# Optimization experiments

Measured on AMD Instinct MI355X. Metric: run time of the kernel, lower is better.

Reference implementation:

```python
import jax, jax.numpy as jnp
import numpy as np

NUM_HEADS = 8


def _mab(Q, K, Wq, bq, Wk, bk, Wv, bv, Wo, bo):
    # MAB with ln=False, dropout=0 (eval). Scale is sqrt(dim_V), matching source.
    B, Lq, _ = Q.shape
    Lk = K.shape[1]
    Dv = Wq.shape[1]
    dh = Dv // NUM_HEADS
    q = (Q @ Wq + bq).reshape(B, Lq, NUM_HEADS, dh).transpose(0, 2, 1, 3)
    k = (K @ Wk + bk).reshape(B, Lk, NUM_HEADS, dh).transpose(0, 2, 1, 3)
    v = (K @ Wv + bv).reshape(B, Lk, NUM_HEADS, dh).transpose(0, 2, 1, 3)
    A = jax.nn.softmax(jnp.einsum('bhqd,bhkd->bhqk', q, k) / jnp.sqrt(jnp.float32(Dv)), axis=-1)
    O = (q + jnp.einsum('bhqk,bhkd->bhqd', A, v)).transpose(0, 2, 1, 3).reshape(B, Lq, Dv)
    return O + jax.nn.relu(O @ Wo + bo)


def _forward(x, adj, gin_W, gin_b, geW1, geb1, geW2, geb2,
             gnW1, gnb1, gnW2, gnb2, goW, gob, S,
             mWq, mbq, mWk, mbk, mWv, mbv, mWo, mbo, finW, finb):
    B, V, T, D = x.shape
    Hd = gin_W.shape[1]
    # --- GNN encoder (adj path) ---
    h = x.reshape(B, V, T * D) @ gin_W + gin_b            # [B,V,H]
    # edge_mlp first linear on cat([h_i,h_j]) == h@Wi (row) + h@Wj (col); avoids 2H concat
    Wi, Wj = geW1[:Hd], geW1[Hd:]
    pre = (h @ Wi)[:, :, None, :] + (h @ Wj)[:, None, :, :] + geb1   # [B,V,V,H]
    e = jax.nn.relu(jax.nn.relu(pre) @ geW2 + geb2)       # [B,V,V,H]
    agg = jnp.einsum('bijh,bij->bih', e, adj)             # mask * sum over j, fused
    node = jax.nn.relu(jax.nn.relu(agg @ gnW1 + gnb1) @ gnW2 + gnb2)
    enc = node @ goW + gob                                # [B,V,H]
    # --- decoder: PMA + SAB + SAB + Linear ---
    o = _mab(jnp.broadcast_to(S, (B,) + S.shape[1:]), enc,
             mWq[0], mbq[0], mWk[0], mbk[0], mWv[0], mbv[0], mWo[0], mbo[0])
    o = _mab(o, o, mWq[1], mbq[1], mWk[1], mbk[1], mWv[1], mbv[1], mWo[1], mbo[1])
    o = _mab(o, o, mWq[2], mbq[2], mWk[2], mbk[2], mWv[2], mbv[2], mWo[2], mbo[2])
    out = o @ finW + finb                                 # [B,num_slots,T*OD]
    return out.reshape(B, S.shape[1], T, finW.shape[1] // T)


def setup_inputs() -> dict:
    key = jax.random.key(0)
    ks = jax.random.split(key, 16)
    B, V, T, D = 4, 256, 12, 4
    H, NS, OD = 256, 16, 32

    def w(k, shape, s=0.02):
        return s * jax.random.normal(k, shape, jnp.float32)

    return {
        'x': jax.random.normal(ks[0], (B, V, T, D), jnp.float32),
        'adj': (jax.random.uniform(ks[1], (B, V, V)) > 0.5).astype(jnp.float32),
        'gin_W': w(ks[2], (T * D, H)), 'gin_b': jnp.zeros((H,), jnp.float32),
        'geW1': w(ks[3], (2 * H, H)), 'geb1': jnp.zeros((H,), jnp.float32),
        'geW2': w(ks[4], (H, H)), 'geb2': jnp.zeros((H,), jnp.float32),
        'gnW1': w(ks[5], (H, H)), 'gnb1': jnp.zeros((H,), jnp.float32),
        'gnW2': w(ks[6], (H, H)), 'gnb2': jnp.zeros((H,), jnp.float32),
        'goW': w(ks[7], (H, H)), 'gob': jnp.zeros((H,), jnp.float32),
        'S': w(ks[8], (1, NS, H), 0.05),
        'mWq': w(ks[9], (3, H, H)), 'mbq': jnp.zeros((3, H), jnp.float32),
        'mWk': w(ks[10], (3, H, H)), 'mbk': jnp.zeros((3, H), jnp.float32),
        'mWv': w(ks[11], (3, H, H)), 'mbv': jnp.zeros((3, H), jnp.float32),
        'mWo': w(ks[12], (3, H, H)), 'mbo': jnp.zeros((3, H), jnp.float32),
        'finW': w(ks[13], (H, T * OD)), 'finb': jnp.zeros((T * OD,), jnp.float32),
    }


def reference(x, adj, gin_W, gin_b, geW1, geb1, geW2, geb2,
              gnW1, gnb1, gnW2, gnb2, goW, gob, S,
              mWq, mbq, mWk, mbk, mWv, mbv, mWo, mbo, finW, finb):
    return _forward(x, adj, gin_W, gin_b, geW1, geb1, geW2, geb2,
                    gnW1, gnb1, gnW2, gnb2, goW, gob, S,
                    mWq, mbq, mWk, mbk, mWv, mbv, mWo, mbo, finW, finb)
```

## Files before the change

### kernel.cpp

```cpp
#include <hip/hip_runtime.h>
#include <hip/hip_bf16.h>

typedef unsigned short u16;
typedef __bf16 bf8v __attribute__((ext_vector_type(8)));
typedef float f4v __attribute__((ext_vector_type(4)));

__device__ __forceinline__ float b2f(u16 v) {
  union { unsigned u; float f; } x; x.u = ((unsigned)v) << 16; return x.f;
}
__device__ __forceinline__ u16 f2b(float f) {
  union { float f; unsigned u; } x; x.f = f;
  unsigned r = (x.u + 0x7FFFu + ((x.u >> 16) & 1u)) >> 16;
  return (u16)r;
}
__device__ __forceinline__ unsigned pkbf(float a, float b) {
  union { __hip_bfloat162 h; unsigned u; } c;
  c.h = __float22bfloat162_rn(make_float2(a, b));
  return c.u;
}
__device__ __forceinline__ void up2(unsigned u, float& lo, float& hi) {
  union { unsigned x; float f; } a, b;
  a.x = u << 16; b.x = u & 0xffff0000u; lo = a.f; hi = b.f;
}

#define NFRAG 19
struct PreArgs {
  const float* fsrc[NFRAG];
  u16* fdst[NFRAG];
  int fstride[NFRAG];
  int fbase[NFRAG + 1];
  int fragTiles, hBase, prepBid, q1Bid;
  const float *x, *ginW, *ginb;
  u16* h_bf;
  const float *mbk, *mbv, *mbq, *S, *mWq;
  float *bkv0, *bqkv1, *bqkv2;
  u16* q1b;
};

__global__ __launch_bounds__(256) void k_pre(PreArgs a) {
  __shared__ u16 ld[256 * 20];
  __shared__ float xs[4][48];
  __shared__ float Ss[4096];
  const int bid = blockIdx.x, t = threadIdx.x;

  if (bid < a.fragTiles) {
    int j = 0;
    while (j + 1 < NFRAG && a.fbase[j + 1] <= bid) j++;
    const int localT = bid - a.fbase[j];
    const float* src = a.fsrc[j];
    const int Ns = a.fstride[j];
    const int n0 = localT * 16;
    {
      const float* s = src + (size_t)t * Ns + n0;
      const float4 v0 = ((const float4*)s)[0], v1 = ((const float4*)s)[1];
      const float4 v2 = ((const float4*)s)[2], v3 = ((const float4*)s)[3];
      unsigned* row = (unsigned*)(ld + t * 20);
      row[0] = pkbf(v0.x, v0.y); row[1] = pkbf(v0.z, v0.w);
      row[2] = pkbf(v1.x, v1.y); row[3] = pkbf(v1.z, v1.w);
      row[4] = pkbf(v2.x, v2.y); row[5] = pkbf(v2.z, v2.w);
      row[6] = pkbf(v3.x, v3.y); row[7] = pkbf(v3.z, v3.w);
    }
    __syncthreads();
    u16* dst = a.fdst[j] + (size_t)localT * 4096;
#pragma unroll
    for (int s2 = 0; s2 < 2; s2++) {
      const int o = t * 2 + s2, kt = o >> 6, lane = o & 63;
      const int nlo = lane & 15, bk = kt * 32 + ((lane >> 4) << 3);
      union { u16 h[8]; uint4 q; } pk;
#pragma unroll
      for (int j2 = 0; j2 < 8; j2++) pk.h[j2] = ld[(bk + j2) * 20 + nlo];
      *(uint4*)(dst + (size_t)(kt * 64 + lane) * 8) = pk.q;
    }
    return;
  }
  if (bid >= a.hBase && bid < a.hBase + 256) {
    const int row0 = (bid - a.hBase) * 4;
    if (t < 192) {
      const int rr = t / 48, k = t % 48;
      xs[rr][k] = a.x[(size_t)(row0 + rr) * 48 + k];
    }
    __syncthreads();
    const float bias = a.ginb[t];
    float acc[4] = {bias, bias, bias, bias};
    for (int k = 0; k < 48; k++) {
      const float w = a.ginW[(size_t)k * 256 + t];
#pragma unroll
      for (int rr = 0; rr < 4; rr++) acc[rr] += xs[rr][k] * w;
    }
#pragma unroll
    for (int rr = 0; rr < 4; rr++) a.h_bf[(size_t)(row0 + rr) * 256 + t] = f2b(acc[rr]);
    return;
  }
  if (bid == a.prepBid) {
    a.bkv0[t] = a.mbk[t]; a.bkv0[256 + t] = a.mbv[t];
    a.bqkv1[t] = a.mbq[256 + t]; a.bqkv1[256 + t] = a.mbk[256 + t]; a.bqkv1[512 + t] = a.mbv[256 + t];
    a.bqkv2[t] = a.mbq[512 + t]; a.bqkv2[256 + t] = a.mbk[512 + t]; a.bqkv2[512 + t] = a.mbv[512 + t];
    return;
  }
  if (bid == a.q1Bid) {
    for (int idx = t; idx < 4096; idx += 256) Ss[idx] = a.S[idx];
    __syncthreads();
    float acc[16];
#pragma unroll
    for (int r = 0; r < 16; r++) acc[r] = 0.f;
    for (int k = 0; k < 256; k++) {
      const float w = a.mWq[(size_t)k * 256 + t];
#pragma unroll
      for (int r = 0; r < 16; r++) acc[r] += Ss[r * 256 + k] * w;
    }
    const float bq = a.mbq[t];
#pragma unroll
    for (int r = 0; r < 16; r++) a.q1b[r * 256 + t] = f2b(acc[r] + bq);
    return;
  }
}

__global__ __launch_bounds__(256) void k_wiwj(
    const u16* __restrict__ h, const u16* __restrict__ frag, float* __restrict__ out) {
  __shared__ __align__(16) u16 As[64 * 264];
  const int t = threadIdx.x, lane = t & 63, wv = t >> 6;
  const int m0 = blockIdx.x * 64, n0 = blockIdx.y * 128;
  {
    const int row = t >> 2, ch = t & 3;
#pragma unroll
    for (int s = 0; s < 8; s++)
      *(uint4*)(As + row * 264 + ch * 64 + s * 8) =
          *(const uint4*)(h + (size_t)(m0 + row) * 256 + ch * 64 + s * 8);
  }
  __syncthreads();
  f4v acc[4][2];
#pragma unroll
  for (int mt = 0; mt < 4; mt++)
#pragma unroll
    for (int nt = 0; nt < 2; nt++) acc[mt][nt] = (f4v){0.f, 0.f, 0.f, 0.f};
  const int Tw = (n0 >> 4) + wv * 2;
#pragma unroll
  for (int kt = 0; kt < 8; kt++) {
    bf8v af[4], bf[2];
#pragma unroll
    for (int mt = 0; mt < 4; mt++)
      af[mt] = *(const bf8v*)(As + (mt * 16 + (lane & 15)) * 264 + kt * 32 + ((lane >> 4) << 3));
#pragma unroll
    for (int nt = 0; nt < 2; nt++)
      bf[nt] = *(const bf8v*)(frag + ((size_t)((Tw + nt) * 8 + kt) * 64 + lane) * 8);
#pragma unroll
    for (int mt = 0; mt < 4; mt++)
#pragma unroll
      for (int nt = 0; nt < 2; nt++)
        acc[mt][nt] = __builtin_amdgcn_mfma_f32_16x16x32_bf16(af[mt], bf[nt], acc[mt][nt], 0, 0, 0);
  }
#pragma unroll
  for (int mt = 0; mt < 4; mt++)
#pragma unroll
    for (int nt = 0; nt < 2; nt++) {
      const int n = n0 + wv * 32 + nt * 16 + (lane & 15);
      const int mb = m0 + mt * 16 + ((lane >> 4) << 2);
#pragma unroll
      for (int r = 0; r < 4; r++) out[(size_t)(mb + r) * 512 + n] = acc[mt][nt][r];
    }
}

__global__ __launch_bounds__(256, 2) void k_edge(
    const float* __restrict__ hWiWj, const float* __restrict__ adj,
    const float* __restrict__ geb1, const u16* __restrict__ fragW2,
    const float* __restrict__ geb2, u16* __restrict__ aggB) {
  __shared__ __align__(16) u16 As[64 * 264];
  __shared__ float hi[256];
  __shared__ int jlist[256];
  __shared__ int cnt;
  const int t = threadIdx.x, lane = t & 63, wv = t >> 6;
  const int b = blockIdx.x >> 8, i = blockIdx.x & 255;
  if (t == 0) cnt = 0;
  __syncthreads();
  {
    const float a = adj[(size_t)(b * 256 + i) * 256 + t];
    hi[t] = hWiWj[(size_t)(b * 256 + i) * 512 + t] + geb1[t];
    if (a != 0.f) { const int p = atomicAdd(&cnt, 1); jlist[p] = t; }
  }
  __syncthreads();
  const int nact = cnt;
  if (nact == 0) {
    if (lane < 16) {
#pragma unroll
      for (int nt = 0; nt < 4; nt++)
        aggB[(size_t)(b * 256 + i) * 256 + wv * 64 + nt * 16 + lane] = 0;
    }
    return;
  }
  const int nch = (nact + 63) >> 6;
  float bias2[4];
#pragma unroll
  for (int nt = 0; nt < 4; nt++) bias2[nt] = geb2[wv * 64 + nt * 16 + (lane & 15)];
  float aggAcc[4] = {0.f, 0.f, 0.f, 0.f};
  const u16* fw = fragW2 + lane * 8;

  for (int c = 0; c < nch; c++) {
    const int rows = min(64, nact - c * 64);
    {
      const int r = t >> 2, q = t & 3;
      const bool valid = (r < rows);
      const int j = valid ? jlist[c * 64 + r] : jlist[0];
      const float4* s4 = (const float4*)(hWiWj + (size_t)(b * 256 + j) * 512 + 256 + q * 64);
      u16* dstrow = As + r * 264 + q * 64;
#pragma unroll
      for (int ii = 0; ii < 8; ii++) {
        const float4 v0 = s4[ii * 2];
        const float4 v1 = s4[ii * 2 + 1];
        const int k = q * 64 + ii * 8;
        uint4 qd;
        qd.x = pkbf(fmaxf(v0.x + hi[k + 0], 0.f), fmaxf(v0.y + hi[k + 1], 0.f));
        qd.y = pkbf(fmaxf(v0.z + hi[k + 2], 0.f), fmaxf(v0.w + hi[k + 3], 0.f));
        qd.z = pkbf(fmaxf(v1.x + hi[k + 4], 0.f), fmaxf(v1.y + hi[k + 5], 0.f));
        qd.w = pkbf(fmaxf(v1.z + hi[k + 6], 0.f), fmaxf(v1.w + hi[k + 7], 0.f));
        *(uint4*)(dstrow + ii * 8) = qd;
      }
    }
    __syncthreads();
    f4v acc[4][4];
#pragma unroll
    for (int jt = 0; jt < 4; jt++)
#pragma unroll
      for (int nt = 0; nt < 4; nt++) acc[jt][nt] = (f4v){0.f, 0.f, 0.f, 0.f};
    bf8v bcur[4];
#pragma unroll
    for (int nt = 0; nt < 4; nt++)
      bcur[nt] = *(const bf8v*)(fw + (size_t)((wv * 4 + nt) * 8 + 0) * 512);
#pragma unroll
    for (int kt = 0; kt < 8; kt++) {
      bf8v bnxt[4];
      if (kt < 7) {
#pragma unroll
        for (int nt = 0; nt < 4; nt++)
          bnxt[nt] = *(const bf8v*)(fw + (size_t)((wv * 4 + nt) * 8 + kt + 1) * 512);
      }
      bf8v af[4];
#pragma unroll
      for (int jt = 0; jt < 4; jt++)
        af[jt] = *(const bf8v*)(As + (jt * 16 + (lane & 15)) * 264 + kt * 32 + ((lane >> 4) << 3));
#pragma unroll
      for (int nt = 0; nt < 4; nt++)
#pragma unroll
        for (int jt = 0; jt < 4; jt++)
          acc[jt][nt] = __builtin_amdgcn_mfma_f32_16x16x32_bf16(af[jt], bcur[nt], acc[jt][nt], 0, 0, 0);
      if (kt < 7) {
#pragma unroll
        for (int nt = 0; nt < 4; nt++) bcur[nt] = bnxt[nt];
      }
    }
    const int rbase = (lane >> 4) * 4;
#pragma unroll
    for (int nt = 0; nt < 4; nt++) {
      float s = 0.f;
#pragma unroll
      for (int jt = 0; jt < 4; jt++) {
        const int r0 = jt * 16 + rbase;
#pragma unroll
        for (int r = 0; r < 4; r++) {
          const float e = fmaxf(acc[jt][nt][r] + bias2[nt], 0.f);
          s += (r0 + r < rows) ? e : 0.f;
        }
      }
      s += __shfl_xor(s, 16);
      s += __shfl_xor(s, 32);
      aggAcc[nt] += s;
    }
    __syncthreads();
  }
  if (lane < 16) {
#pragma unroll
    for (int nt = 0; nt < 4; nt++) {
      const int n = wv * 64 + nt * 16 + lane;
      aggB[(size_t)(b * 256 + i) * 256 + n] = f2b(aggAcc[nt]);
    }
  }
}

#define NBLK 32

__device__ __forceinline__ void gridbar(int* cnt, int gen) {
  __syncthreads();
  if (threadIdx.x == 0) {
    __threadfence();
    __hip_atomic_fetch_add(cnt, 1, __ATOMIC_RELAXED, __HIP_MEMORY_SCOPE_AGENT);
    int it = 0;
    while (__hip_atomic_load(cnt, __ATOMIC_RELAXED, __HIP_MEMORY_SCOPE_AGENT) < NBLK * gen) {
      __builtin_amdgcn_s_sleep(8);
      if (((++it) & 255) == 0)
        __hip_atomic_fetch_add(cnt, 0, __ATOMIC_RELAXED, __HIP_MEMORY_SCOPE_AGENT);
    }
    __threadfence();
  }
  __syncthreads();
}

__device__ void g32(const u16* Al, const u16* frag, const float* bias, int relu,
                    u16* Ol, int t) {
  const int lane = t & 63, wv = t >> 6;
  f4v acc[2][4];
#pragma unroll
  for (int mt = 0; mt < 2; mt++)
#pragma unroll
    for (int nt = 0; nt < 4; nt++) acc[mt][nt] = (f4v){0.f, 0.f, 0.f, 0.f};
#pragma unroll
  for (int kt = 0; kt < 8; kt++) {
    bf8v af[2], bf[4];
#pragma unroll
    for (int mt = 0; mt < 2; mt++)
      af[mt] = *(const bf8v*)(Al + (mt * 16 + (lane & 15)) * 264 + kt * 32 + ((lane >> 4) << 3));
#pragma unroll
    for (int nt = 0; nt < 4; nt++)
      bf[nt] = *(const bf8v*)(frag + ((size_t)((wv * 4 + nt) * 8 + kt) * 64 + lane) * 8);
#pragma unroll
    for (int mt = 0; mt < 2; mt++)
#pragma unroll
      for (int nt = 0; nt < 4; nt++)
        acc[mt][nt] = __builtin_amdgcn_mfma_f32_16x16x32_bf16(af[mt], bf[nt], acc[mt][nt], 0, 0, 0);
  }
#pragma unroll
  for (int mt = 0; mt < 2; mt++)
#pragma unroll
    for (int nt = 0; nt < 4; nt++) {
      const int col = wv * 64 + nt * 16 + (lane & 15);
      const float bv = bias[col];
#pragma unroll
      for (int r = 0; r < 4; r++) {
        const int row = mt * 16 + ((lane >> 4) << 2) + r;
        float v = acc[mt][nt][r] + bv;
        if (relu) v = fmaxf(v, 0.f);
        Ol[row * 264 + col] = f2b(v);
      }
    }
}

__device__ void g32kv(const u16* Al, const u16* frag, const float* bias,
                      u16* outG, int t) {
  const int lane = t & 63, wv = t >> 6;
  f4v acc[2][8];
#pragma unroll
  for (int mt = 0; mt < 2; mt++)
#pragma unroll
    for (int nt = 0; nt < 8; nt++) acc[mt][nt] = (f4v){0.f, 0.f, 0.f, 0.f};
#pragma unroll
  for (int kt = 0; kt < 8; kt++) {
    bf8v af[2];
#pragma unroll
    for (int mt = 0; mt < 2; mt++)
      af[mt] = *(const bf8v*)(Al + (mt * 16 + (lane & 15)) * 264 + kt * 32 + ((lane >> 4) << 3));
#pragma unroll
    for (int nt = 0; nt < 8; nt++) {
      const bf8v bf = *(const bf8v*)(frag + ((size_t)((wv * 8 + nt) * 8 + kt) * 64 + lane) * 8);
#pragma unroll
      for (int mt = 0; mt < 2; mt++)
        acc[mt][nt] = __builtin_amdgcn_mfma_f32_16x16x32_bf16(af[mt], bf, acc[mt][nt], 0, 0, 0);
    }
  }
#pragma unroll
  for (int mt = 0; mt < 2; mt++)
#pragma unroll
    for (int nt = 0; nt < 8; nt++) {
      const int col = wv * 128 + nt * 16 + (lane & 15);
      const float bv = bias[col];
#pragma unroll
      for (int r = 0; r < 4; r++) {
        const int row = mt * 16 + ((lane >> 4) << 2) + r;
        outG[(size_t)row * 512 + col] = f2b(acc[mt][nt][r] + bv);
      }
    }
}

__device__ void wproj(const u16* __restrict__ actA, const float* __restrict__ residG,
                      const u16* __restrict__ frag, const float* __restrict__ bias,
                      int mode, u16* __restrict__ outBf, float* __restrict__ outF,
                      int Nout, int b, int T, int lane) {
  f4v acc = (f4v){0.f, 0.f, 0.f, 0.f};
  const u16* abase = actA + (size_t)(b * 16 + (lane & 15)) * 256 + ((lane >> 4) << 3);
  const u16* fbase = frag + ((size_t)(T * 8) * 64 + lane) * 8;
#pragma unroll
  for (int kt = 0; kt < 8; kt++) {
    const bf8v af = *(const bf8v*)(abase + kt * 32);
    const bf8v bf = *(const bf8v*)(fbase + (size_t)kt * 512);
    acc = __builtin_amdgcn_mfma_f32_16x16x32_bf16(af, bf, acc, 0, 0, 0);
  }
  const int col = T * 16 + (lane & 15);
  const float bv = bias[col];
#pragma unroll
  for (int r = 0; r < 4; r++) {
    const int row = b * 16 + ((lane >> 4) << 2) + r;
    float v = acc[r] + bv;
    if (mode == 1) v = fmaxf(v, 0.f) + residG[(size_t)row * 256 + col];
    if (outBf) outBf[(size_t)row * Nout + col] = f2b(v);
    if (outF) outF[(size_t)row * Nout + col] = v;
  }
}

__device__ void wattn(const u16* __restrict__ qkvG, float* __restrict__ attF,
                      u16* __restrict__ attB, float* psW, int b, int hd, int lane) {
  const int r = lane & 15, cg = lane >> 4;
  float qv[32];
  {
    const uint4* qp = (const uint4*)(qkvG + (size_t)(b * 16 + r) * 768 + hd * 32);
#pragma unroll
    for (int c4 = 0; c4 < 4; c4++) {
      const uint4 q4 = qp[c4];
      up2(q4.x, qv[c4 * 8 + 0], qv[c4 * 8 + 1]);
      up2(q4.y, qv[c4 * 8 + 2], qv[c4 * 8 + 3]);
      up2(q4.z, qv[c4 * 8 + 4], qv[c4 * 8 + 5]);
      up2(q4.w, qv[c4 * 8 + 6], qv[c4 * 8 + 7]);
    }
  }
  float p[4];
#pragma unroll
  for (int c = 0; c < 4; c++) {
    const int cc = cg * 4 + c;
    const uint4* kp = (const uint4*)(qkvG + (size_t)(b * 16 + cc) * 768 + 256 + hd * 32);
    float s = 0.f;
#pragma unroll
    for (int c4 = 0; c4 < 4; c4++) {
      const uint4 k4 = kp[c4];
      float k0, k1;
      up2(k4.x, k0, k1); s += qv[c4 * 8 + 0] * k0 + qv[c4 * 8 + 1] * k1;
      up2(k4.y, k0, k1); s += qv[c4 * 8 + 2] * k0 + qv[c4 * 8 + 3] * k1;
      up2(k4.z, k0, k1); s += qv[c4 * 8 + 4] * k0 + qv[c4 * 8 + 5] * k1;
      up2(k4.w, k0, k1); s += qv[c4 * 8 + 6] * k0 + qv[c4 * 8 + 7] * k1;
    }
    p[c] = s * 0.0625f;
  }
  float mx = fmaxf(fmaxf(p[0], p[1]), fmaxf(p[2], p[3]));
  mx = fmaxf(mx, __shfl_xor(mx, 16));
  mx = fmaxf(mx, __shfl_xor(mx, 32));
  float sum = 0.f;
#pragma unroll
  for (int c = 0; c < 4; c++) { p[c] = __expf(p[c] - mx); sum += p[c]; }
  sum += __shfl_xor(sum, 16);
  sum += __shfl_xor(sum, 32);
  const float inv = 1.f / sum;
#pragma unroll
  for (int c = 0; c < 4; c++) psW[r * 16 + cg * 4 + c] = p[c] * inv;
  float o[8];
#pragma unroll
  for (int j = 0; j < 8; j++) o[j] = qv[cg * 8 + j];
#pragma unroll
  for (int c = 0; c < 16; c++) {
    const float pv = psW[r * 16 + c];
    const uint4 v4 = *(const uint4*)(qkvG + (size_t)(b * 16 + c) * 768 + 512 + hd * 32 + cg * 8);
    float v0, v1;
    up2(v4.x, v0, v1); o[0] += pv * v0; o[1] += pv * v1;
    up2(v4.y, v0, v1); o[2] += pv * v0; o[3] += pv * v1;
    up2(v4.z, v0, v1); o[4] += pv * v0; o[5] += pv * v1;
    up2(v4.w, v0, v1); o[6] += pv * v0; o[7] += pv * v1;
  }
  const int row = b * 16 + r, col0 = hd * 32 + cg * 8;
#pragma unroll
  for (int j = 0; j < 8; j++) attF[(size_t)row * 256 + col0 + j] = o[j];
  unsigned* ob = (unsigned*)(attB + (size_t)row * 256 + col0);
  ob[0] = pkbf(o[0], o[1]); ob[1] = pkbf(o[2], o[3]);
  ob[2] = pkbf(o[4], o[5]); ob[3] = pkbf(o[6], o[7]);
}

__device__ void attn_tile(const u16* __restrict__ qbuf, int qshared,
                          const u16* __restrict__ kbuf, const u16* __restrict__ vbuf,
                          float* __restrict__ oF, u16* __restrict__ oB,
                          int b, int hd, float* qs, float* sc, float* vs, int t) {
  const int lane = t & 63, wv = t >> 6;
  const int Lk = 256;
  if (t < 64) {
    const int row = t >> 2, part = t & 3;
    const int qrow = qshared ? row : (b * 16 + row);
    const uint4 q4 = *(const uint4*)(qbuf + (size_t)qrow * 256 + hd * 32 + part * 8);
    float f0, f1, f2, f3, f4, f5, f6, f7;
    up2(q4.x, f0, f1); up2(q4.y, f2, f3); up2(q4.z, f4, f5); up2(q4.w, f6, f7);
    float4* d = (float4*)(qs + row * 32 + part * 8);
    d[0] = make_float4(f0, f1, f2, f3);
    d[1] = make_float4(f4, f5, f6, f7);
  }
  __syncthreads();
  {
    float kv[32];
    const uint4* kp = (const uint4*)(kbuf + (size_t)(b * Lk + t) * 512 + hd * 32);
#pragma unroll
    for (int c4 = 0; c4 < 4; c4++) {
      const uint4 k4 = kp[c4];
      up2(k4.x, kv[c4 * 8 + 0], kv[c4 * 8 + 1]);
      up2(k4.y, kv[c4 * 8 + 2], kv[c4 * 8 + 3]);
      up2(k4.z, kv[c4 * 8 + 4], kv[c4 * 8 + 5]);
      up2(k4.w, kv[c4 * 8 + 6], kv[c4 * 8 + 7]);
    }
    for (int r = 0; r < 16; r++) {
      float s = 0.f;
#pragma unroll
      for (int d = 0; d < 32; d++) s += qs[r * 32 + d] * kv[d];
      sc[r * 256 + t] = s * 0.0625f;
    }
  }
  __syncthreads();
  for (int r = wv * 4; r < wv * 4 + 4; r++) {
    float v[4];
    float mx = -1e30f;
#pragma unroll
    for (int q2 = 0; q2 < 4; q2++) {
      v[q2] = sc[r * 256 + lane + q2 * 64];
      mx = fmaxf(mx, v[q2]);
    }
    for (int off = 32; off; off >>= 1) mx = fmaxf(mx, __shfl_xor(mx, off));
    float sum = 0.f;
#pragma unroll
    for (int q2 = 0; q2 < 4; q2++) { v[q2] = __expf(v[q2] - mx); sum += v[q2]; }
    for (int off = 32; off; off >>= 1) sum += __shfl_xor(sum, off);
    const float inv = 1.f / sum;
#pragma unroll
    for (int q2 = 0; q2 < 4; q2++) sc[r * 256 + lane + q2 * 64] = v[q2] * inv;
  }
  __syncthreads();
  for (int u = t; u < 1024; u += 256) {
    const int row = u >> 2, part = u & 3;
    const uint4 v4 = *(const uint4*)(vbuf + (size_t)(b * Lk + row) * 512 + hd * 32 + part * 8);
    float f0, f1, f2, f3, f4, f5, f6, f7;
    up2(v4.x, f0, f1); up2(v4.y, f2, f3); up2(v4.z, f4, f5); up2(v4.w, f6, f7);
    float4* d = (float4*)(vs + row * 32 + part * 8);
    d[0] = make_float4(f0, f1, f2, f3);
    d[1] = make_float4(f4, f5, f6, f7);
  }
  __syncthreads();
  const int r0 = t >> 5, d = t & 31;
  float a0 = qs[r0 * 32 + d], a1 = qs[(r0 + 8) * 32 + d];
#pragma unroll 4
  for (int j = 0; j < Lk; j++) {
    const float vv = vs[j * 32 + d];
    a0 += sc[r0 * 256 + j] * vv;
    a1 += sc[(r0 + 8) * 256 + j] * vv;
  }
  const int c0 = hd * 32 + d;
  oF[(size_t)(b * 16 + r0) * 256 + c0] = a0;
  oB[(size_t)(b * 16 + r0) * 256 + c0] = f2b(a0);
  oF[(size_t)(b * 16 + r0 + 8) * 256 + c0] = a1;
  oB[(size_t)(b * 16 + r0 + 8) * 256 + c0] = f2b(a1);
}

struct TailArgs {
  const u16 *agg, *fGn1, *fGn2, *fGo, *fKV0, *fQKV1, *fQKV2, *fO0, *fO1, *fO2, *fFin, *q1b;
  const float *gnb1, *gnb2, *gob, *bkv0, *bqkv1, *bqkv2, *mbo, *finb;
  u16 *kv1, *o1b, *actBf, *qkvG, *attB;
  float *o1f, *attF, *outF;
  int* bar;
};

__global__ __launch_bounds__(256) void k_tail(TailArgs a) {
  __shared__ __align__(16) char smem[51200];
  const int bid = blockIdx.x, t = threadIdx.x;
  const int lane = t & 63;
  const int wid = bid * 4 + (t >> 6);

  {
    u16* actA = (u16*)smem;
    u16* actB = (u16*)(smem + 16896);
    const int r0 = bid * 32;
#pragma unroll
    for (int s = 0; s < 4; s++) {
      const int u = t * 4 + s, row = u >> 5, ch = u & 31;
      *(uint4*)(actA + row * 264 + ch * 8) =
          *(const uint4*)(a.agg + (size_t)(r0 + row) * 256 + ch * 8);
    }
    __syncthreads();
    g32(actA, a.fGn1, a.gnb1, 1, actB, t); __syncthreads();
    g32(actB, a.fGn2, a.gnb2, 1, actA, t); __syncthreads();
    g32(actA, a.fGo, a.gob, 0, actB, t); __syncthreads();
    g32kv(actB, a.fKV0, a.bkv0, a.kv1 + (size_t)r0 * 512, t);
  }
  gridbar(a.bar, 1);
  {
    float* qs = (float*)smem;
    float* sc = (float*)(smem + 2048);
    float* vs = (float*)(smem + 18432);
    attn_tile(a.q1b, 1, a.kv1, a.kv1 + 256, a.o1f, a.o1b, bid >> 3, bid & 7, qs, sc, vs, t);
  }
  gridbar(a.bar, 2);
  float* psW = (float*)smem + (t >> 6) * 256;
  if (wid < 64) wproj(a.o1b, a.o1f, a.fO0, a.mbo, 1, a.actBf, nullptr, 256, wid >> 4, wid & 15, lane);
  gridbar(a.bar, 3);
  for (int u = wid; u < 192; u += 128)
    wproj(a.actBf, nullptr, a.fQKV1, a.bqkv1, 0, a.qkvG, nullptr, 768, u / 48, u % 48, lane);
  gridbar(a.bar, 4);
  if (wid < 32) wattn(a.qkvG, a.attF, a.attB, psW, wid >> 3, wid & 7, lane);
  gridbar(a.bar, 5);
  if (wid < 64) wproj(a.attB, a.attF, a.fO1, a.mbo + 256, 1, a.actBf, nullptr, 256, wid >> 4, wid & 15, lane);
  gridbar(a.bar, 6);
  for (int u = wid; u < 192; u += 128)
    wproj(a.actBf, nullptr, a.fQKV2, a.bqkv2, 0, a.qkvG, nullptr, 768, u / 48, u % 48, lane);
  gridbar(a.bar, 7);
  if (wid < 32) wattn(a.qkvG, a.attF, a.attB, psW, wid >> 3, wid & 7, lane);
  gridbar(a.bar, 8);
  if (wid < 64) wproj(a.attB, a.attF, a.fO2, a.mbo + 512, 1, a.actBf, nullptr, 256, wid >> 4, wid & 15, lane);
  gridbar(a.bar, 9);
  if (wid < 96) wproj(a.actBf, nullptr, a.fFin, a.finb, 0, nullptr, a.outF, 384, wid / 24, wid % 24, lane);
}

extern "C" void kernel_launch(void* const* d_in, const int* in_sizes, int n_in,
                              void* d_out, int out_size, void* d_ws, size_t ws_size,
                              hipStream_t stream) {
  const float* x    = (const float*)d_in[0];
  const float* adj  = (const float*)d_in[1];
  const float* ginW = (const float*)d_in[2];
  const float* ginb = (const float*)d_in[3];
  const float* geW1 = (const float*)d_in[4];
  const float* geb1 = (const float*)d_in[5];
  const float* geW2 = (const float*)d_in[6];
  const float* geb2 = (const float*)d_in[7];
  const float* gnW1 = (const float*)d_in[8];
  const float* gnb1 = (const float*)d_in[9];
  const float* gnW2 = (const float*)d_in[10];
  const float* gnb2 = (const float*)d_in[11];
  const float* goW  = (const float*)d_in[12];
  const float* gob  = (const float*)d_in[13];
  const float* S    = (const float*)d_in[14];
  const float* mWq  = (const float*)d_in[15];
  const float* mbq  = (const float*)d_in[16];
  const float* mWk  = (const float*)d_in[17];
  const float* mbk  = (const float*)d_in[18];
  const float* mWv  = (const float*)d_in[19];
  const float* mbv  = (const float*)d_in[20];
  const float* mWo  = (const float*)d_in[21];
  const float* mbo  = (const float*)d_in[22];
  const float* finW = (const float*)d_in[23];
  const float* finb = (const float*)d_in[24];
  (void)in_sizes; (void)n_in; (void)out_size; (void)ws_size;

  char* wp = (char*)d_ws;
  size_t off = 0;
  auto alloc = [&](size_t bytes) -> char* {
    char* p = wp + off;
    off += (bytes + 255) & ~(size_t)255;
    return p;
  };
  u16* h_bf     = (u16*)alloc(1024 * 256 * 2);
  float* hWiWjf = (float*)alloc((size_t)1024 * 512 * 4);
  u16* fWiWj    = (u16*)alloc(512 * 256 * 2);
  u16* fW2      = (u16*)alloc(256 * 256 * 2);
  u16* fGn1     = (u16*)alloc(256 * 256 * 2);
  u16* fGn2     = (u16*)alloc(256 * 256 * 2);
  u16* fGo      = (u16*)alloc(256 * 256 * 2);
  u16* fQ0      = (u16*)alloc(256 * 256 * 2);
  u16* fKV0     = (u16*)alloc(512 * 256 * 2);
  u16* fQKV1    = (u16*)alloc(768 * 256 * 2);
  u16* fQKV2    = (u16*)alloc(768 * 256 * 2);
  u16* fO0      = (u16*)alloc(256 * 256 * 2);
  u16* fO1      = (u16*)alloc(256 * 256 * 2);
  u16* fO2      = (u16*)alloc(256 * 256 * 2);
  u16* fFin     = (u16*)alloc(384 * 256 * 2);
  float* bkv0   = (float*)alloc(512 * 4);
  float* bqkv1  = (float*)alloc(768 * 4);
  float* bqkv2  = (float*)alloc(768 * 4);
  u16* q1b      = (u16*)alloc(16 * 256 * 2);
  u16* agg_b    = (u16*)alloc(1024 * 256 * 2);
  u16* kv1      = (u16*)alloc(1024 * 512 * 2);
  float* o1f    = (float*)alloc(64 * 256 * 4);
  u16* o1b      = (u16*)alloc(64 * 256 * 2);
  u16* actBf    = (u16*)alloc(64 * 256 * 2);
  u16* qkvG     = (u16*)alloc(64 * 768 * 2);
  float* attF   = (float*)alloc(64 * 256 * 4);
  u16* attB     = (u16*)alloc(64 * 256 * 2);
  int* bar      = (int*)alloc(256);

  PreArgs P{};
  int nj = 0, tiles = 0;
  auto addF = [&](const float* s, int stride, u16* d, int nT) {
    P.fsrc[nj] = s; P.fdst[nj] = d; P.fstride[nj] = stride; P.fbase[nj] = tiles;
    tiles += nT; nj++;
  };
  addF(geW1, 256, fWiWj, 16);
  addF(geW1 + 65536, 256, fWiWj + 16 * 4096, 16);
  addF(geW2, 256, fW2, 16);
  addF(gnW1, 256, fGn1, 16);
  addF(gnW2, 256, fGn2, 16);
  addF(goW, 256, fGo, 16);
  addF(mWq, 256, fQ0, 16);
  addF(mWk, 256, fKV0, 16);
  addF(mWv, 256, fKV0 + 16 * 4096, 16);
  addF(mWq + 65536, 256, fQKV1, 16);
  addF(mWk + 65536, 256, fQKV1 + 16 * 4096, 16);
  addF(mWv + 65536, 256, fQKV1 + 32 * 4096, 16);
  addF(mWq + 131072, 256, fQKV2, 16);
  addF(mWk + 131072, 256, fQKV2 + 16 * 4096, 16);
  addF(mWv + 131072, 256, fQKV2 + 32 * 4096, 16);
  addF(mWo, 256, fO0, 16);
  addF(mWo + 65536, 256, fO1, 16);
  addF(mWo + 131072, 256, fO2, 16);
  addF(finW, 384, fFin, 24);
  P.fbase[nj] = tiles;
  P.fragTiles = tiles;
  P.hBase = tiles;
  P.prepBid = tiles + 256;
  P.q1Bid = tiles + 257;
  P.x = x; P.ginW = ginW; P.ginb = ginb; P.h_bf = h_bf;
  P.mbk = mbk; P.mbv = mbv; P.mbq = mbq; P.S = S; P.mWq = mWq;
  P.bkv0 = bkv0; P.bqkv1 = bqkv1; P.bqkv2 = bqkv2; P.q1b = q1b;

  TailArgs T{};
  T.agg = agg_b; T.fGn1 = fGn1; T.fGn2 = fGn2; T.fGo = fGo; T.fKV0 = fKV0;
  T.fQKV1 = fQKV1; T.fQKV2 = fQKV2; T.fO0 = fO0; T.fO1 = fO1; T.fO2 = fO2;
  T.fFin = fFin; T.q1b = q1b;
  T.gnb1 = gnb1; T.gnb2 = gnb2; T.gob = gob;
  T.bkv0 = bkv0; T.bqkv1 = bqkv1; T.bqkv2 = bqkv2; T.mbo = mbo; T.finb = finb;
  T.kv1 = kv1; T.o1b = o1b; T.actBf = actBf; T.qkvG = qkvG; T.attB = attB;
  T.o1f = o1f; T.attF = attF; T.outF = (float*)d_out;
  T.bar = bar;

  hipMemsetAsync(bar, 0, 256, stream);
  k_pre<<<dim3(tiles + 258), dim3(256), 0, stream>>>(P);
  k_wiwj<<<dim3(16, 4), dim3(256), 0, stream>>>(h_bf, fWiWj, hWiWjf);
  k_edge<<<dim3(1024), dim3(256), 0, stream>>>(hWiWjf, adj, geb1, fW2, geb2, agg_b);
  k_tail<<<dim3(NBLK), dim3(256), 0, stream>>>(T);
}
```

Before: 266.0 us.

## Replace grid-barrier tail with per-batch 1024-thread blocks using shared memory

The tail kernel drops its 32-block layout and the nine software grid barriers in favour of one 1024-thread block per batch element. Activations, QKV, residuals and attention probabilities now live in shared memory, so only __syncthreads separates the decoder stages and the global scratch round trips go away. The attention V tile is kept in shared memory as bf16 rather than fp32 to fit the budget. k_edge's launch bounds are also raised from 2 to 3 blocks per CU. The cost is that the tail now runs on only 4 CUs, which cuts parallelism in the GNN MLP and KV stages, and it needs 136 KB of shared memory per block.

```diff
diff --git a/kernel.cpp b/kernel.cpp
--- a/kernel.cpp
+++ b/kernel.cpp
@@ -160,7 +160,7 @@
     }
 }
 
-__global__ __launch_bounds__(256, 2) void k_edge(
+__global__ __launch_bounds__(256, 3) void k_edge(
     const float* __restrict__ hWiWj, const float* __restrict__ adj,
     const float* __restrict__ geb1, const u16* __restrict__ fragW2,
     const float* __restrict__ geb2, u16* __restrict__ aggB) {
@@ -275,23 +275,6 @@
   }
 }
 
-#define NBLK 32
-
-__device__ __forceinline__ void gridbar(int* cnt, int gen) {
-  __syncthreads();
-  if (threadIdx.x == 0) {
-    __threadfence();
-    __hip_atomic_fetch_add(cnt, 1, __ATOMIC_RELAXED, __HIP_MEMORY_SCOPE_AGENT);
-    int it = 0;
-    while (__hip_atomic_load(cnt, __ATOMIC_RELAXED, __HIP_MEMORY_SCOPE_AGENT) < NBLK * gen) {
-      __builtin_amdgcn_s_sleep(8);
-      if (((++it) & 255) == 0)
-        __hip_atomic_fetch_add(cnt, 0, __ATOMIC_RELAXED, __HIP_MEMORY_SCOPE_AGENT);
-    }
-    __threadfence();
-  }
-  __syncthreads();
-}
 
 __device__ void g32(const u16* Al, const u16* frag, const float* bias, int relu,
                     u16* Ol, int t) {
@@ -368,37 +351,162 @@
     }
 }
 
-__device__ void wproj(const u16* __restrict__ actA, const float* __restrict__ residG,
-                      const u16* __restrict__ frag, const float* __restrict__ bias,
-                      int mode, u16* __restrict__ outBf, float* __restrict__ outF,
-                      int Nout, int b, int T, int lane) {
+__device__ void attn_squad(const u16* __restrict__ q1b, const u16* __restrict__ kv1,
+                           float* __restrict__ o1f, u16* __restrict__ o1b,
+                           int b, int hd, float* qs, float* sc, u16* vsB, int st) {
+  const int lane = st & 63, wv = st >> 6;
+  if (st < 64) {
+    const int row = st >> 2, part = st & 3;
+    const uint4 q4 = *(const uint4*)(q1b + (size_t)row * 256 + hd * 32 + part * 8);
+    float f0, f1, f2, f3, f4, f5, f6, f7;
+    up2(q4.x, f0, f1); up2(q4.y, f2, f3); up2(q4.z, f4, f5); up2(q4.w, f6, f7);
+    float4* d = (float4*)(qs + row * 32 + part * 8);
+    d[0] = make_float4(f0, f1, f2, f3);
+    d[1] = make_float4(f4, f5, f6, f7);
+  }
+  for (int idx = st; idx < 1024; idx += 256) {
+    const int row = idx >> 2, part = idx & 3;
+    *(uint4*)(vsB + row * 32 + part * 8) =
+        *(const uint4*)(kv1 + (size_t)(b * 256 + row) * 512 + 256 + hd * 32 + part * 8);
+  }
+  __syncthreads();
+  {
+    float kv[32];
+    const uint4* kp = (const uint4*)(kv1 + (size_t)(b * 256 + st) * 512 + hd * 32);
+#pragma unroll
+    for (int c4 = 0; c4 < 4; c4++) {
+      const uint4 k4 = kp[c4];
+      up2(k4.x, kv[c4 * 8 + 0], kv[c4 * 8 + 1]);
+      up2(k4.y, kv[c4 * 8 + 2], kv[c4 * 8 + 3]);
+      up2(k4.z, kv[c4 * 8 + 4], kv[c4 * 8 + 5]);
+      up2(k4.w, kv[c4 * 8 + 6], kv[c4 * 8 + 7]);
+    }
+    for (int r = 0; r < 16; r++) {
+      float s = 0.f;
+#pragma unroll
+      for (int d = 0; d < 32; d++) s += qs[r * 32 + d] * kv[d];
+      sc[r * 256 + st] = s * 0.0625f;
+    }
+  }
+  __syncthreads();
+  for (int r = wv * 4; r < wv * 4 + 4; r++) {
+    float v[4];
+    float mx = -1e30f;
+#pragma unroll
+    for (int q2 = 0; q2 < 4; q2++) {
+      v[q2] = sc[r * 256 + lane + q2 * 64];
+      mx = fmaxf(mx, v[q2]);
+    }
+    for (int off = 32; off; off >>= 1) mx = fmaxf(mx, __shfl_xor(mx, off));
+    float sum = 0.f;
+#pragma unroll
+    for (int q2 = 0; q2 < 4; q2++) { v[q2] = __expf(v[q2] - mx); sum += v[q2]; }
+    for (int off = 32; off; off >>= 1) sum += __shfl_xor(sum, off);
+    const float inv = 1.f / sum;
+#pragma unroll
+    for (int q2 = 0; q2 < 4; q2++) sc[r * 256 + lane + q2 * 64] = v[q2] * inv;
+  }
+  __syncthreads();
+  const int r0 = st >> 5, d = st & 31;
+  float a0 = qs[r0 * 32 + d], a1 = qs[(r0 + 8) * 32 + d];
+#pragma unroll 4
+  for (int j = 0; j < 256; j++) {
+    const float vv = b2f(vsB[j * 32 + d]);
+    a0 += sc[r0 * 256 + j] * vv;
+    a1 += sc[(r0 + 8) * 256 + j] * vv;
+  }
+  const int c0 = hd * 32 + d;
+  o1f[(size_t)(b * 16 + r0) * 256 + c0] = a0;
+  o1b[(size_t)(b * 16 + r0) * 256 + c0] = f2b(a0);
+  o1f[(size_t)(b * 16 + r0 + 8) * 256 + c0] = a1;
+  o1b[(size_t)(b * 16 + r0 + 8) * 256 + c0] = f2b(a1);
+}
+
+__device__ void wprojG(const u16* __restrict__ o1b, const float* __restrict__ o1f,
+                       const u16* __restrict__ frag, const float* __restrict__ bias,
+                       u16* actL, float* residL, int b, int T, int lane) {
   f4v acc = (f4v){0.f, 0.f, 0.f, 0.f};
-  const u16* abase = actA + (size_t)(b * 16 + (lane & 15)) * 256 + ((lane >> 4) << 3);
+  const u16* abase = o1b + (size_t)(b * 16 + (lane & 15)) * 256 + ((lane >> 4) << 3);
   const u16* fbase = frag + ((size_t)(T * 8) * 64 + lane) * 8;
 #pragma unroll
-  for (int kt = 0; kt < 8; kt++) {
-    const bf8v af = *(const bf8v*)(abase + kt * 32);
-    const bf8v bf = *(const bf8v*)(fbase + (size_t)kt * 512);
-    acc = __builtin_amdgcn_mfma_f32_16x16x32_bf16(af, bf, acc, 0, 0, 0);
-  }
+  for (int kt = 0; kt < 8; kt++)
+    acc = __builtin_amdgcn_mfma_f32_16x16x32_bf16(*(const bf8v*)(abase + kt * 32),
+                                                  *(const bf8v*)(fbase + (size_t)kt * 512), acc, 0, 0, 0);
   const int col = T * 16 + (lane & 15);
   const float bv = bias[col];
 #pragma unroll
   for (int r = 0; r < 4; r++) {
-    const int row = b * 16 + ((lane >> 4) << 2) + r;
-    float v = acc[r] + bv;
-    if (mode == 1) v = fmaxf(v, 0.f) + residG[(size_t)row * 256 + col];
-    if (outBf) outBf[(size_t)row * Nout + col] = f2b(v);
-    if (outF) outF[(size_t)row * Nout + col] = v;
-  }
-}
-
-__device__ void wattn(const u16* __restrict__ qkvG, float* __restrict__ attF,
-                      u16* __restrict__ attB, float* psW, int b, int hd, int lane) {
+    const int row = ((lane >> 4) << 2) + r;
+    const float v = fmaxf(acc[r] + bv, 0.f) + o1f[(size_t)(b * 16 + row) * 256 + col];
+    residL[row * 256 + col] = v;
+    actL[row * 264 + col] = f2b(v);
+  }
+}
+
+__device__ void wprojQ(const u16* actL, const u16* __restrict__ frag,
+                       const float* __restrict__ bias, u16* qkvL, int T, int lane) {
+  f4v acc = (f4v){0.f, 0.f, 0.f, 0.f};
+  const u16* abase = actL + (lane & 15) * 264 + ((lane >> 4) << 3);
+  const u16* fbase = frag + ((size_t)(T * 8) * 64 + lane) * 8;
+#pragma unroll
+  for (int kt = 0; kt < 8; kt++)
+    acc = __builtin_amdgcn_mfma_f32_16x16x32_bf16(*(const bf8v*)(abase + kt * 32),
+                                                  *(const bf8v*)(fbase + (size_t)kt * 512), acc, 0, 0, 0);
+  const int col = T * 16 + (lane & 15);
+  const float bv = bias[col];
+#pragma unroll
+  for (int r = 0; r < 4; r++) {
+    const int row = ((lane >> 4) << 2) + r;
+    qkvL[row * 776 + col] = f2b(acc[r] + bv);
+  }
+}
+
+__device__ void wprojR(const u16* actIn, const u16* __restrict__ frag,
+                       const float* __restrict__ bias, u16* actOut, float* residL,
+                       int T, int lane) {
+  f4v acc = (f4v){0.f, 0.f, 0.f, 0.f};
+  const u16* abase = actIn + (lane & 15) * 264 + ((lane >> 4) << 3);
+  const u16* fbase = frag + ((size_t)(T * 8) * 64 + lane) * 8;
+#pragma unroll
+  for (int kt = 0; kt < 8; kt++)
+    acc = __builtin_amdgcn_mfma_f32_16x16x32_bf16(*(const bf8v*)(abase + kt * 32),
+                                                  *(const bf8v*)(fbase + (size_t)kt * 512), acc, 0, 0, 0);
+  const int col = T * 16 + (lane & 15);
+  const float bv = bias[col];
+#pragma unroll
+  for (int r = 0; r < 4; r++) {
+    const int row = ((lane >> 4) << 2) + r;
+    const float v = fmaxf(acc[r] + bv, 0.f) + residL[row * 256 + col];
+    residL[row * 256 + col] = v;
+    actOut[row * 264 + col] = f2b(v);
+  }
+}
+
+__device__ void wprojF(const u16* actL, const u16* __restrict__ frag,
+                       const float* __restrict__ bias, float* __restrict__ outG,
+                       int T, int lane) {
+  f4v acc = (f4v){0.f, 0.f, 0.f, 0.f};
+  const u16* abase = actL + (lane & 15) * 264 + ((lane >> 4) << 3);
+  const u16* fbase = frag + ((size_t)(T * 8) * 64 + lane) * 8;
+#pragma unroll
+  for (int kt = 0; kt < 8; kt++)
+    acc = __builtin_amdgcn_mfma_f32_16x16x32_bf16(*(const bf8v*)(abase + kt * 32),
+                                                  *(const bf8v*)(fbase + (size_t)kt * 512), acc, 0, 0, 0);
+  const int col = T * 16 + (lane & 15);
+  const float bv = bias[col];
+#pragma unroll
+  for (int r = 0; r < 4; r++) {
+    const int row = ((lane >> 4) << 2) + r;
+    outG[(size_t)row * 384 + col] = acc[r] + bv;
+  }
+}
+
+__device__ void attnB(const u16* qkvL, float* residL, u16* actOut, float* ps,
+                      int hd, int lane) {
   const int r = lane & 15, cg = lane >> 4;
   float qv[32];
   {
-    const uint4* qp = (const uint4*)(qkvG + (size_t)(b * 16 + r) * 768 + hd * 32);
+    const uint4* qp = (const uint4*)(qkvL + r * 776 + hd * 32);
 #pragma unroll
     for (int c4 = 0; c4 < 4; c4++) {
       const uint4 q4 = qp[c4];
@@ -412,7 +520,7 @@
 #pragma unroll
   for (int c = 0; c < 4; c++) {
     const int cc = cg * 4 + c;
-    const uint4* kp = (const uint4*)(qkvG + (size_t)(b * 16 + cc) * 768 + 256 + hd * 32);
+    const uint4* kp = (const uint4*)(qkvL + cc * 776 + 256 + hd * 32);
     float s = 0.f;
 #pragma unroll
     for (int c4 = 0; c4 < 4; c4++) {
@@ -435,163 +543,91 @@
   sum += __shfl_xor(sum, 32);
   const float inv = 1.f / sum;
 #pragma unroll
-  for (int c = 0; c < 4; c++) psW[r * 16 + cg * 4 + c] = p[c] * inv;
+  for (int c = 0; c < 4; c++) ps[r * 16 + cg * 4 + c] = p[c] * inv;
   float o[8];
 #pragma unroll
   for (int j = 0; j < 8; j++) o[j] = qv[cg * 8 + j];
 #pragma unroll
   for (int c = 0; c < 16; c++) {
-    const float pv = psW[r * 16 + c];
-    const uint4 v4 = *(const uint4*)(qkvG + (size_t)(b * 16 + c) * 768 + 512 + hd * 32 + cg * 8);
+    const float pv = ps[r * 16 + c];
+    const uint4 v4 = *(const uint4*)(qkvL + c * 776 + 512 + hd * 32 + cg * 8);
     float v0, v1;
     up2(v4.x, v0, v1); o[0] += pv * v0; o[1] += pv * v1;
     up2(v4.y, v0, v1); o[2] += pv * v0; o[3] += pv * v1;
     up2(v4.z, v0, v1); o[4] += pv * v0; o[5] += pv * v1;
     up2(v4.w, v0, v1); o[6] += pv * v0; o[7] += pv * v1;
   }
-  const int row = b * 16 + r, col0 = hd * 32 + cg * 8;
-#pragma unroll
-  for (int j = 0; j < 8; j++) attF[(size_t)row * 256 + col0 + j] = o[j];
-  unsigned* ob = (unsigned*)(attB + (size_t)row * 256 + col0);
+  const int col0 = hd * 32 + cg * 8;
+#pragma unroll
+  for (int j = 0; j < 8; j++) residL[r * 256 + col0 + j] = o[j];
+  unsigned* ob = (unsigned*)(actOut + r * 264 + col0);
   ob[0] = pkbf(o[0], o[1]); ob[1] = pkbf(o[2], o[3]);
   ob[2] = pkbf(o[4], o[5]); ob[3] = pkbf(o[6], o[7]);
-}
-
-__device__ void attn_tile(const u16* __restrict__ qbuf, int qshared,
-                          const u16* __restrict__ kbuf, const u16* __restrict__ vbuf,
-                          float* __restrict__ oF, u16* __restrict__ oB,
-                          int b, int hd, float* qs, float* sc, float* vs, int t) {
-  const int lane = t & 63, wv = t >> 6;
-  const int Lk = 256;
-  if (t < 64) {
-    const int row = t >> 2, part = t & 3;
-    const int qrow = qshared ? row : (b * 16 + row);
-    const uint4 q4 = *(const uint4*)(qbuf + (size_t)qrow * 256 + hd * 32 + part * 8);
-    float f0, f1, f2, f3, f4, f5, f6, f7;
-    up2(q4.x, f0, f1); up2(q4.y, f2, f3); up2(q4.z, f4, f5); up2(q4.w, f6, f7);
-    float4* d = (float4*)(qs + row * 32 + part * 8);
-    d[0] = make_float4(f0, f1, f2, f3);
-    d[1] = make_float4(f4, f5, f6, f7);
-  }
-  __syncthreads();
-  {
-    float kv[32];
-    const uint4* kp = (const uint4*)(kbuf + (size_t)(b * Lk + t) * 512 + hd * 32);
-#pragma unroll
-    for (int c4 = 0; c4 < 4; c4++) {
-      const uint4 k4 = kp[c4];
-      up2(k4.x, kv[c4 * 8 + 0], kv[c4 * 8 + 1]);
-      up2(k4.y, kv[c4 * 8 + 2], kv[c4 * 8 + 3]);
-      up2(k4.z, kv[c4 * 8 + 4], kv[c4 * 8 + 5]);
-      up2(k4.w, kv[c4 * 8 + 6], kv[c4 * 8 + 7]);
-    }
-    for (int r = 0; r < 16; r++) {
-      float s = 0.f;
-#pragma unroll
-      for (int d = 0; d < 32; d++) s += qs[r * 32 + d] * kv[d];
-      sc[r * 256 + t] = s * 0.0625f;
-    }
-  }
-  __syncthreads();
-  for (int r = wv * 4; r < wv * 4 + 4; r++) {
-    float v[4];
-    float mx = -1e30f;
-#pragma unroll
-    for (int q2 = 0; q2 < 4; q2++) {
-      v[q2] = sc[r * 256 + lane + q2 * 64];
-      mx = fmaxf(mx, v[q2]);
-    }
-    for (int off = 32; off; off >>= 1) mx = fmaxf(mx, __shfl_xor(mx, off));
-    float sum = 0.f;
-#pragma unroll
-    for (int q2 = 0; q2 < 4; q2++) { v[q2] = __expf(v[q2] - mx); sum += v[q2]; }
-    for (int off = 32; off; off >>= 1) sum += __shfl_xor(sum, off);
-    const float inv = 1.f / sum;
-#pragma unroll
-    for (int q2 = 0; q2 < 4; q2++) sc[r * 256 + lane + q2 * 64] = v[q2] * inv;
-  }
-  __syncthreads();
-  for (int u = t; u < 1024; u += 256) {
-    const int row = u >> 2, part = u & 3;
-    const uint4 v4 = *(const uint4*)(vbuf + (size_t)(b * Lk + row) * 512 + hd * 32 + part * 8);
-    float f0, f1, f2, f3, f4, f5, f6, f7;
-    up2(v4.x, f0, f1); up2(v4.y, f2, f3); up2(v4.z, f4, f5); up2(v4.w, f6, f7);
-    float4* d = (float4*)(vs + row * 32 + part * 8);
-    d[0] = make_float4(f0, f1, f2, f3);
-    d[1] = make_float4(f4, f5, f6, f7);
-  }
-  __syncthreads();
-  const int r0 = t >> 5, d = t & 31;
-  float a0 = qs[r0 * 32 + d], a1 = qs[(r0 + 8) * 32 + d];
-#pragma unroll 4
-  for (int j = 0; j < Lk; j++) {
-    const float vv = vs[j * 32 + d];
-    a0 += sc[r0 * 256 + j] * vv;
-    a1 += sc[(r0 + 8) * 256 + j] * vv;
-  }
-  const int c0 = hd * 32 + d;
-  oF[(size_t)(b * 16 + r0) * 256 + c0] = a0;
-  oB[(size_t)(b * 16 + r0) * 256 + c0] = f2b(a0);
-  oF[(size_t)(b * 16 + r0 + 8) * 256 + c0] = a1;
-  oB[(size_t)(b * 16 + r0 + 8) * 256 + c0] = f2b(a1);
 }
 
 struct TailArgs {
   const u16 *agg, *fGn1, *fGn2, *fGo, *fKV0, *fQKV1, *fQKV2, *fO0, *fO1, *fO2, *fFin, *q1b;
   const float *gnb1, *gnb2, *gob, *bkv0, *bqkv1, *bqkv2, *mbo, *finb;
-  u16 *kv1, *o1b, *actBf, *qkvG, *attB;
-  float *o1f, *attF, *outF;
-  int* bar;
+  u16 *kv1, *o1b;
+  float *o1f, *outF;
 };
 
-__global__ __launch_bounds__(256) void k_tail(TailArgs a) {
-  __shared__ __align__(16) char smem[51200];
-  const int bid = blockIdx.x, t = threadIdx.x;
-  const int lane = t & 63;
-  const int wid = bid * 4 + (t >> 6);
+__global__ __launch_bounds__(1024) void k_tail(TailArgs a) {
+  __shared__ __align__(16) char smem[139264];
+  const int b = blockIdx.x, t = threadIdx.x;
+  const int sq = t >> 8, st = t & 255;
+  const int lane = t & 63, w = t >> 6;
 
   {
-    u16* actA = (u16*)smem;
-    u16* actB = (u16*)(smem + 16896);
-    const int r0 = bid * 32;
-#pragma unroll
-    for (int s = 0; s < 4; s++) {
-      const int u = t * 4 + s, row = u >> 5, ch = u & 31;
-      *(uint4*)(actA + row * 264 + ch * 8) =
-          *(const uint4*)(a.agg + (size_t)(r0 + row) * 256 + ch * 8);
-    }
-    __syncthreads();
-    g32(actA, a.fGn1, a.gnb1, 1, actB, t); __syncthreads();
-    g32(actB, a.fGn2, a.gnb2, 1, actA, t); __syncthreads();
-    g32(actA, a.fGo, a.gob, 0, actB, t); __syncthreads();
-    g32kv(actB, a.fKV0, a.bkv0, a.kv1 + (size_t)r0 * 512, t);
-  }
-  gridbar(a.bar, 1);
+    u16* act0 = (u16*)(smem + sq * 33792);
+    u16* act1 = act0 + 8448;
+    for (int c = 0; c < 2; c++) {
+      const int r0 = b * 256 + (sq + 4 * c) * 32;
+#pragma unroll
+      for (int s = 0; s < 4; s++) {
+        const int u = st * 4 + s, row = u >> 5, ch = u & 31;
+        *(uint4*)(act0 + row * 264 + ch * 8) =
+            *(const uint4*)(a.agg + (size_t)(r0 + row) * 256 + ch * 8);
+      }
+      __syncthreads();
+      g32(act0, a.fGn1, a.gnb1, 1, act1, st); __syncthreads();
+      g32(act1, a.fGn2, a.gnb2, 1, act0, st); __syncthreads();
+      g32(act0, a.fGo, a.gob, 0, act1, st); __syncthreads();
+      g32kv(act1, a.fKV0, a.bkv0, a.kv1 + (size_t)r0 * 512, st);
+      __syncthreads();
+    }
+  }
   {
-    float* qs = (float*)smem;
-    float* sc = (float*)(smem + 2048);
-    float* vs = (float*)(smem + 18432);
-    attn_tile(a.q1b, 1, a.kv1, a.kv1 + 256, a.o1f, a.o1b, bid >> 3, bid & 7, qs, sc, vs, t);
-  }
-  gridbar(a.bar, 2);
-  float* psW = (float*)smem + (t >> 6) * 256;
-  if (wid < 64) wproj(a.o1b, a.o1f, a.fO0, a.mbo, 1, a.actBf, nullptr, 256, wid >> 4, wid & 15, lane);
-  gridbar(a.bar, 3);
-  for (int u = wid; u < 192; u += 128)
-    wproj(a.actBf, nullptr, a.fQKV1, a.bqkv1, 0, a.qkvG, nullptr, 768, u / 48, u % 48, lane);
-  gridbar(a.bar, 4);
-  if (wid < 32) wattn(a.qkvG, a.attF, a.attB, psW, wid >> 3, wid & 7, lane);
-  gridbar(a.bar, 5);
-  if (wid < 64) wproj(a.attB, a.attF, a.fO1, a.mbo + 256, 1, a.actBf, nullptr, 256, wid >> 4, wid & 15, lane);
-  gridbar(a.bar, 6);
-  for (int u = wid; u < 192; u += 128)
-    wproj(a.actBf, nullptr, a.fQKV2, a.bqkv2, 0, a.qkvG, nullptr, 768, u / 48, u % 48, lane);
-  gridbar(a.bar, 7);
-  if (wid < 32) wattn(a.qkvG, a.attF, a.attB, psW, wid >> 3, wid & 7, lane);
-  gridbar(a.bar, 8);
-  if (wid < 64) wproj(a.attB, a.attF, a.fO2, a.mbo + 512, 1, a.actBf, nullptr, 256, wid >> 4, wid & 15, lane);
-  gridbar(a.bar, 9);
-  if (wid < 96) wproj(a.actBf, nullptr, a.fFin, a.finb, 0, nullptr, a.outF, 384, wid / 24, wid % 24, lane);
+    float* qs = (float*)(smem + sq * 34816);
+    float* sc = (float*)(smem + sq * 34816 + 2048);
+    u16* vsB = (u16*)(smem + sq * 34816 + 18432);
+    for (int c = 0; c < 2; c++) {
+      attn_squad(a.q1b, a.kv1, a.o1f, a.o1b, b, sq * 2 + c, qs, sc, vsB, st);
+      __syncthreads();
+    }
+  }
+  u16* act0 = (u16*)smem;
+  u16* act1 = (u16*)(smem + 8448);
+  u16* qkvL = (u16*)(smem + 16896);
+  float* residL = (float*)(smem + 41728);
+  float* psL = (float*)(smem + 58112);
+
+  wprojG(a.o1b, a.o1f, a.fO0, a.mbo, act0, residL, b, w, lane);
+  __syncthreads();
+  for (int T = w; T < 48; T += 16) wprojQ(act0, a.fQKV1, a.bqkv1, qkvL, T, lane);
+  __syncthreads();
+  if (w < 8) attnB(qkvL, residL, act1, psL + w * 256, w, lane);
+  __syncthreads();
+  wprojR(act1, a.fO1, a.mbo + 256, act0, residL, w, lane);
+  __syncthreads();
+  for (int T = w; T < 48; T += 16) wprojQ(act0, a.fQKV2, a.bqkv2, qkvL, T, lane);
+  __syncthreads();
+  if (w < 8) attnB(qkvL, residL, act1, psL + w * 256, w, lane);
+  __syncthreads();
+  wprojR(act1, a.fO2, a.mbo + 512, act0, residL, w, lane);
+  __syncthreads();
+  for (int T = w; T < 24; T += 16)
+    wprojF(act0, a.fFin, a.finb, a.outF + (size_t)b * 16 * 384, T, lane);
 }
 
 extern "C" void kernel_launch(void* const* d_in, const int* in_sizes, int n_in,
@@ -654,11 +690,6 @@
   u16* kv1      = (u16*)alloc(1024 * 512 * 2);
   float* o1f    = (float*)alloc(64 * 256 * 4);
   u16* o1b      = (u16*)alloc(64 * 256 * 2);
-  u16* actBf    = (u16*)alloc(64 * 256 * 2);
-  u16* qkvG     = (u16*)alloc(64 * 768 * 2);
-  float* attF   = (float*)alloc(64 * 256 * 4);
-  u16* attB     = (u16*)alloc(64 * 256 * 2);
-  int* bar      = (int*)alloc(256);
 
   PreArgs P{};
   int nj = 0, tiles = 0;
@@ -700,13 +731,10 @@
   T.fFin = fFin; T.q1b = q1b;
   T.gnb1 = gnb1; T.gnb2 = gnb2; T.gob = gob;
   T.bkv0 = bkv0; T.bqkv1 = bqkv1; T.bqkv2 = bqkv2; T.mbo = mbo; T.finb = finb;
-  T.kv1 = kv1; T.o1b = o1b; T.actBf = actBf; T.qkvG = qkvG; T.attB = attB;
-  T.o1f = o1f; T.attF = attF; T.outF = (float*)d_out;
-  T.bar = bar;
-
-  hipMemsetAsync(bar, 0, 256, stream);
+  T.kv1 = kv1; T.o1b = o1b; T.o1f = o1f; T.outF = (float*)d_out;
+
   k_pre<<<dim3(tiles + 258), dim3(256), 0, stream>>>(P);
   k_wiwj<<<dim3(16, 4), dim3(256), 0, stream>>>(h_bf, fWiWj, hWiWjf);
   k_edge<<<dim3(1024), dim3(256), 0, stream>>>(hWiWjf, adj, geb1, fW2, geb2, agg_b);
-  k_tail<<<dim3(NBLK), dim3(256), 0, stream>>>(T);
-}
+  k_tail<<<dim3(4), dim3(1024), 0, stream>>>(T);
+}
```

After: 520.2 us. 1.96x slower.
